# Optimization experiments

Hardware: AMD Instinct MI355X
Metric: run time of the kernel (lower is better)

Reference implementation:

```python
import jax, jax.numpy as jnp
import numpy as np

N_NODES = 50000

def setup_inputs() -> dict:
    key = jax.random.key(0)
    ks = jax.random.split(key, 8)
    d_in, d_h = 128, 128
    x = jax.random.normal(ks[0], (N_NODES, d_in), dtype=jnp.float32)
    edge_index = jax.random.randint(ks[1], (2, 800000), 0, N_NODES, dtype=jnp.int64)
    edge_pairs = jax.random.randint(ks[2], (1000000, 2), 0, N_NODES, dtype=jnp.int64)
    W_gcn = jax.random.normal(ks[3], (d_in, d_h), dtype=jnp.float32) / np.sqrt(d_in)
    b_gcn = jnp.zeros((d_h,), dtype=jnp.float32)
    W1 = jax.random.normal(ks[4], (2 * d_h, d_h), dtype=jnp.float32) / np.sqrt(2 * d_h)
    b1 = jnp.zeros((d_h,), dtype=jnp.float32)
    W2 = jax.random.normal(ks[5], (d_h, 1), dtype=jnp.float32) / np.sqrt(d_h)
    b2 = jnp.zeros((1,), dtype=jnp.float32)
    return {"x": x, "edge_index": edge_index, "edge_pairs": edge_pairs,
            "W_gcn": W_gcn, "b_gcn": b_gcn, "W1": W1, "b1": b1, "W2": W2, "b2": b2}

def gcn_conv(x, edge_index, W, b):
    # PyG GCNConv default: add self-loops, symmetric normalization.
    n = x.shape[0]
    loop = jnp.arange(n, dtype=edge_index.dtype)
    src = jnp.concatenate([edge_index[0], loop])  # [E+N]
    dst = jnp.concatenate([edge_index[1], loop])
    deg = jax.ops.segment_sum(jnp.ones(src.shape[0], dtype=x.dtype), dst, num_segments=n)
    dinv = jnp.where(deg > 0, jax.lax.rsqrt(deg), 0.0)
    norm = dinv[src] * dinv[dst]                  # [E+N]
    h = x @ W                                     # [N, H]
    agg = jax.ops.segment_sum(h[src] * norm[:, None], dst, num_segments=n)
    return agg + b

def reference(x, edge_index, edge_pairs, W_gcn, b_gcn, W1, b1, W2, b2):
    h = gcn_conv(x, edge_index, W_gcn, b_gcn)      # [N, H]
    e = jnp.concatenate([h[edge_pairs[:, 0]], h[edge_pairs[:, 1]]], axis=-1)  # [P, 2H]
    edge_logits = jax.nn.relu(e @ W1 + b1) @ W2 + b2  # [P, 1]
    return edge_logits, edge_pairs, h
```

## Files before the change

kernel.cpp:

```cpp
#include <hip/hip_runtime.h>
#include <hip/hip_fp16.h>

#define WG 256

typedef _Float16 f16;
typedef _Float16 hv2 __attribute__((ext_vector_type(2)));
typedef _Float16 f16x4 __attribute__((ext_vector_type(4)));
typedef _Float16 f16x8 __attribute__((ext_vector_type(8)));
typedef float f32x4 __attribute__((ext_vector_type(4)));

__global__ __launch_bounds__(WG) void k_misc0(const float* __restrict__ Wg,
                                              f16* __restrict__ Wgt,
                                              const float* __restrict__ W1,
                                              f16* __restrict__ W1t) {
    int b = blockIdx.x;
    if (b < 64) {
        int i = b * WG + threadIdx.x;
        int k = i & 127, nI = i >> 7;
        Wgt[i] = (f16)Wg[(size_t)k * 128 + nI];
    } else {
        int i = (b - 64) * WG + threadIdx.x;
        int k = i & 255, nI = i >> 8;
        W1t[i] = (f16)W1[(size_t)k * 128 + nI];
    }
}

__global__ __launch_bounds__(WG) void k_fusedA(const float* __restrict__ A,
                                               const f16* __restrict__ Wt,
                                               __half2* __restrict__ Out, int n,
                                               const int* __restrict__ dst,
                                               int* __restrict__ deg,
                                               int* __restrict__ rank, int e,
                                               const int* __restrict__ pairs,
                                               float* __restrict__ outp, int n4,
                                               int nmm, int necnt, int ncvt) {
    __shared__ __align__(16) char smem[64 * 136 * 2 + 128 * 136 * 2];
    int b = blockIdx.x, slot = b & 3, idx = b >> 2;
    int tid = threadIdx.x;
    if (slot == 1 || slot == 3) {
        int hid = idx * 2 + (slot >> 1);
        if (hid >= necnt) return;
        int i = hid * WG + tid;
        if (i < e) rank[i] = atomicAdd(&deg[dst[i]], 1);
        return;
    }
    if (slot == 2) {
        if (idx >= ncvt) return;
        int i = idx * WG + tid;
        if (i < n4) {
            int4 v = ((const int4*)pairs)[i];
            ((float4*)outp)[i] = make_float4((float)v.x, (float)v.y, (float)v.z, (float)v.w);
        }
        return;
    }
    if (idx >= nmm) return;
    f16(*As)[136] = (f16(*)[136])smem;
    f16(*Bs)[136] = (f16(*)[136])(smem + 64 * 136 * 2);
    const int row0 = idx * 64;
    for (int f = tid; f < 128 * 16; f += WG) {
        int r = f >> 4, c = f & 15;
        *(float4*)&Bs[r][c * 8] = ((const float4*)Wt)[r * 16 + c];
    }
    for (int f = tid; f < 64 * 32; f += WG) {
        int r = f >> 5, c = f & 31;
        float4 v = make_float4(0.f, 0.f, 0.f, 0.f);
        if (row0 + r < n) v = ((const float4*)A)[(size_t)(row0 + r) * 32 + c];
        *(f16x4*)&As[r][c * 4] = (f16x4){(f16)v.x, (f16)v.y, (f16)v.z, (f16)v.w};
    }
    __syncthreads();
    const int wv = tid >> 6, lane = tid & 63, m = lane & 15, quad = lane >> 4;
    f32x4 acc[8];
#pragma unroll
    for (int t = 0; t < 8; ++t) acc[t] = (f32x4){0.f, 0.f, 0.f, 0.f};
#pragma unroll
    for (int kk = 0; kk < 4; ++kk) {
        f16x8 af = *(f16x8*)&As[wv * 16 + m][kk * 32 + quad * 8];
#pragma unroll
        for (int t = 0; t < 8; ++t) {
            f16x8 bf = *(f16x8*)&Bs[t * 16 + m][kk * 32 + quad * 8];
            acc[t] = __builtin_amdgcn_mfma_f32_16x16x32_f16(af, bf, acc[t], 0, 0, 0);
        }
    }
#pragma unroll
    for (int r = 0; r < 4; ++r) {
        int row = row0 + wv * 16 + quad * 4 + r;
        if (row < n) {
#pragma unroll
            for (int t = 0; t < 4; ++t)
                Out[(size_t)row * 64 + t * 16 + m] =
                    __floats2half2_rn(acc[t][r], acc[t + 4][r]);
        }
    }
}

__global__ __launch_bounds__(WG) void k_scan1(const int* __restrict__ deg,
                                              float* __restrict__ dinv,
                                              int* __restrict__ base,
                                              int* __restrict__ bsum, int n) {
    __shared__ int t[WG];
    int tid = threadIdx.x;
    int i = blockIdx.x * WG + tid;
    int v = (i < n) ? deg[i] : 0;
    if (i < n) dinv[i] = rsqrtf((float)(v + 1));
    t[tid] = v;
    __syncthreads();
    for (int o = 1; o < WG; o <<= 1) {
        int add = (tid >= o) ? t[tid - o] : 0;
        __syncthreads();
        t[tid] += add;
        __syncthreads();
    }
    if (i < n) base[i] = t[tid] - v;
    if (tid == WG - 1) bsum[blockIdx.x] = t[WG - 1];
}

__global__ __launch_bounds__(WG) void k_scan23(int* __restrict__ base,
                                               const int* __restrict__ bsum,
                                               int n, int e, int nb) {
    __shared__ int t[WG];
    int tid = threadIdx.x;
    int v = (tid < nb) ? bsum[tid] : 0;
    t[tid] = v;
    __syncthreads();
    for (int o = 1; o < WG; o <<= 1) {
        int add = (tid >= o) ? t[tid - o] : 0;
        __syncthreads();
        t[tid] += add;
        __syncthreads();
    }
    int off = t[blockIdx.x] - ((blockIdx.x < nb) ? bsum[blockIdx.x] : 0);
    int i = blockIdx.x * WG + tid;
    if (i < n) {
        base[i] += off;
        if (i == n - 1) base[n] = e;
    }
}

__global__ __launch_bounds__(WG) void k_fill(const int* __restrict__ src,
                                             const int* __restrict__ dst,
                                             const int* __restrict__ base,
                                             const int* __restrict__ rank,
                                             int* __restrict__ esrc, int e) {
    int i = blockIdx.x * WG + threadIdx.x;
    if (i >= e) return;
    esrc[base[dst[i]] + rank[i]] = src[i];
}

__global__ __launch_bounds__(WG) void k_gather(const __half2* __restrict__ Hpk,
                                               const float* __restrict__ dinv,
                                               const float* __restrict__ bg,
                                               const int* __restrict__ base,
                                               const int* __restrict__ esrc,
                                               float* __restrict__ outh, int n) {
    int tid = threadIdx.x;
    int node = blockIdx.x * 16 + (tid >> 4);
    int sub = tid & 15;
    if (node >= n) return;
    float dv = dinv[node];
    int4 hh = *(const int4*)(Hpk + (size_t)node * 64 + 4 * sub);
    const int* hp = (const int*)&hh;
    float accl[4], acch[4];
#pragma unroll
    for (int k = 0; k < 4; ++k) {
        hv2 h = __builtin_bit_cast(hv2, hp[k]);
        accl[k] = (float)h[0] * dv;
        acch[k] = (float)h[1] * dv;
    }
    const int j = base[node], jend = base[node + 1];
    for (int j0 = j; j0 < jend; j0 += 8) {
        int s[8];
#pragma unroll
        for (int t = 0; t < 8; ++t) {
            int jt = j0 + t;
            s[t] = esrc[jt < jend ? jt : jend - 1];
        }
        float ds[8];
#pragma unroll
        for (int t = 0; t < 8; ++t) ds[t] = (j0 + t < jend) ? dinv[s[t]] : 0.f;
        int4 r[8];
#pragma unroll
        for (int t = 0; t < 8; ++t)
            r[t] = *(const int4*)(Hpk + (size_t)s[t] * 64 + 4 * sub);
#pragma unroll
        for (int t = 0; t < 8; ++t) {
            const int* pr = (const int*)&r[t];
#pragma unroll
            for (int k = 0; k < 4; ++k) {
                hv2 h = __builtin_bit_cast(hv2, pr[k]);
                accl[k] = fmaf((float)h[0], ds[t], accl[k]);
                acch[k] = fmaf((float)h[1], ds[t], acch[k]);
            }
        }
    }
    float4 blo = *(const float4*)(bg + 4 * sub);
    float4 bhi = *(const float4*)(bg + 4 * sub + 64);
    *(float4*)&outh[(size_t)node * 128 + 4 * sub] =
        make_float4(fmaf(accl[0], dv, blo.x), fmaf(accl[1], dv, blo.y),
                    fmaf(accl[2], dv, blo.z), fmaf(accl[3], dv, blo.w));
    *(float4*)&outh[(size_t)node * 128 + 64 + 4 * sub] =
        make_float4(fmaf(acch[0], dv, bhi.x), fmaf(acch[1], dv, bhi.y),
                    fmaf(acch[2], dv, bhi.z), fmaf(acch[3], dv, bhi.w));
}

__global__ __launch_bounds__(WG) void k_mm_uv(const float* __restrict__ A,
                                              const f16* __restrict__ W1t,
                                              const float* __restrict__ b1,
                                              __half2* __restrict__ Up,
                                              __half2* __restrict__ Vp, int n) {
    __shared__ f16 As[64][136];
    __shared__ f16 Bs[128][136];
    const int tid = threadIdx.x;
    const int row0 = blockIdx.x * 64;
    for (int f = tid; f < 64 * 32; f += WG) {
        int r = f >> 5, c = f & 31;
        float4 v = make_float4(0.f, 0.f, 0.f, 0.f);
        if (row0 + r < n) v = ((const float4*)A)[(size_t)(row0 + r) * 32 + c];
        *(f16x4*)&As[r][c * 4] = (f16x4){(f16)v.x, (f16)v.y, (f16)v.z, (f16)v.w};
    }
    const int wv = tid >> 6, lane = tid & 63, m = lane & 15, quad = lane >> 4;
    f32x4 acc[8];
#pragma unroll
    for (int ph = 0; ph < 2; ++ph) {
        if (ph) __syncthreads();
        for (int f = tid; f < 128 * 16; f += WG) {
            int r = f >> 4, c = f & 15;
            *(float4*)&Bs[r][c * 8] = *(const float4*)(W1t + (size_t)r * 256 + ph * 128 + c * 8);
        }
        __syncthreads();
#pragma unroll
        for (int t = 0; t < 8; ++t) acc[t] = (f32x4){0.f, 0.f, 0.f, 0.f};
#pragma unroll
        for (int kk = 0; kk < 4; ++kk) {
            f16x8 af = *(f16x8*)&As[wv * 16 + m][kk * 32 + quad * 8];
#pragma unroll
            for (int t = 0; t < 8; ++t) {
                f16x8 bf = *(f16x8*)&Bs[t * 16 + m][kk * 32 + quad * 8];
                acc[t] = __builtin_amdgcn_mfma_f32_16x16x32_f16(af, bf, acc[t], 0, 0, 0);
            }
        }
        __half2* Out = ph ? Vp : Up;
#pragma unroll
        for (int t = 0; t < 4; ++t) {
            float bl = 0.f, bh = 0.f;
            if (!ph) { bl = b1[t * 16 + m]; bh = b1[t * 16 + m + 64]; }
#pragma unroll
            for (int r = 0; r < 4; ++r) {
                int row = row0 + wv * 16 + quad * 4 + r;
                if (row < n)
                    Out[(size_t)row * 64 + t * 16 + m] =
                        __floats2half2_rn(acc[t][r] + bl, acc[t + 4][r] + bh);
            }
        }
    }
}

__global__ __launch_bounds__(WG) void k_pair16(const __half2* __restrict__ U,
                                               const __half2* __restrict__ V,
                                               const float* __restrict__ W2,
                                               const float* __restrict__ b2,
                                               const int* __restrict__ pairs,
                                               float* __restrict__ out_logit, int p) {
    int wv = (blockIdx.x * WG + threadIdx.x) >> 6;
    int lane = threadIdx.x & 63;
    int g = lane >> 4, sub = lane & 15;
    int qb = wv * 16 + g;
    if (qb >= p) return;
    int q0 = qb;
    int q1 = (qb + 4 < p) ? qb + 4 : qb;
    int q2 = (qb + 8 < p) ? qb + 8 : qb;
    int q3 = (qb + 12 < p) ? qb + 12 : qb;
    int a0 = pairs[2 * q0], b0 = pairs[2 * q0 + 1];
    int a1 = pairs[2 * q1], b1i = pairs[2 * q1 + 1];
    int a2 = pairs[2 * q2], b2i = pairs[2 * q2 + 1];
    int a3 = pairs[2 * q3], b3i = pairs[2 * q3 + 1];

    int4 u0 = *(const int4*)(U + (size_t)a0 * 64 + 4 * sub);
    int4 v0 = *(const int4*)(V + (size_t)b0 * 64 + 4 * sub);
    int4 u1 = *(const int4*)(U + (size_t)a1 * 64 + 4 * sub);
    int4 v1 = *(const int4*)(V + (size_t)b1i * 64 + 4 * sub);
    int4 u2 = *(const int4*)(U + (size_t)a2 * 64 + 4 * sub);
    int4 v2 = *(const int4*)(V + (size_t)b2i * 64 + 4 * sub);
    int4 u3 = *(const int4*)(U + (size_t)a3 * 64 + 4 * sub);
    int4 v3 = *(const int4*)(V + (size_t)b3i * 64 + 4 * sub);

    float4 w2lo = ((const float4*)W2)[sub];
    float4 w2hi = ((const float4*)(W2 + 64))[sub];
    hv2 w2h[4];
    w2h[0] = hv2{(f16)w2lo.x, (f16)w2hi.x};
    w2h[1] = hv2{(f16)w2lo.y, (f16)w2hi.y};
    w2h[2] = hv2{(f16)w2lo.z, (f16)w2hi.z};
    w2h[3] = hv2{(f16)w2lo.w, (f16)w2hi.w};

    const int* ui0 = (const int*)&u0;
    const int* vi0 = (const int*)&v0;
    const int* ui1 = (const int*)&u1;
    const int* vi1 = (const int*)&v1;
    const int* ui2 = (const int*)&u2;
    const int* vi2 = (const int*)&v2;
    const int* ui3 = (const int*)&u3;
    const int* vi3 = (const int*)&v3;

    const hv2 z2 = hv2{(f16)0.f, (f16)0.f};
    float p0 = 0.f, p1 = 0.f, p2 = 0.f, p3 = 0.f;
#pragma unroll
    for (int k = 0; k < 4; ++k) {
        hv2 s0 = __builtin_bit_cast(hv2, ui0[k]) + __builtin_bit_cast(hv2, vi0[k]);
        hv2 s1 = __builtin_bit_cast(hv2, ui1[k]) + __builtin_bit_cast(hv2, vi1[k]);
        hv2 s2 = __builtin_bit_cast(hv2, ui2[k]) + __builtin_bit_cast(hv2, vi2[k]);
        hv2 s3 = __builtin_bit_cast(hv2, ui3[k]) + __builtin_bit_cast(hv2, vi3[k]);
        p0 = __builtin_amdgcn_fdot2(__builtin_elementwise_max(s0, z2), w2h[k], p0, false);
        p1 = __builtin_amdgcn_fdot2(__builtin_elementwise_max(s1, z2), w2h[k], p1, false);
        p2 = __builtin_amdgcn_fdot2(__builtin_elementwise_max(s2, z2), w2h[k], p2, false);
        p3 = __builtin_amdgcn_fdot2(__builtin_elementwise_max(s3, z2), w2h[k], p3, false);
    }
#pragma unroll
    for (int m = 1; m < 16; m <<= 1) {
        p0 += __shfl_xor(p0, m, 64);
        p1 += __shfl_xor(p1, m, 64);
        p2 += __shfl_xor(p2, m, 64);
        p3 += __shfl_xor(p3, m, 64);
    }
    if (sub == 0) {
        float bb = b2[0];
        out_logit[q0] = p0 + bb;
        if (qb + 4 < p) out_logit[qb + 4] = p1 + bb;
        if (qb + 8 < p) out_logit[qb + 8] = p2 + bb;
        if (qb + 12 < p) out_logit[qb + 12] = p3 + bb;
    }
}

extern "C" void kernel_launch(void* const* d_in, const int* in_sizes, int n_in,
                              void* d_out, int out_size, void* d_ws, size_t ws_size,
                              hipStream_t stream) {
    const float* x     = (const float*)d_in[0];
    const int*   eidx  = (const int*)d_in[1];
    const int*   pairs = (const int*)d_in[2];
    const float* W_gcn = (const float*)d_in[3];
    const float* b_gcn = (const float*)d_in[4];
    const float* W1    = (const float*)d_in[5];
    const float* b1    = (const float*)d_in[6];
    const float* W2    = (const float*)d_in[7];
    const float* b2    = (const float*)d_in[8];

    const int N = in_sizes[0] / 128;
    const int E = in_sizes[1] / 2;
    const int P = in_sizes[2] / 2;
    const int* esrc_in = eidx;
    const int* edst_in = eidx + E;

    float* ws      = (float*)d_ws;
    int*   deg     = (int*)d_ws;
    float* dinv    = ws + 65536;
    int*   base    = (int*)(ws + 131072);
    int*   bsum    = (int*)(ws + 196608);
    f16*   Wt_gcn  = (f16*)(ws + 197120);
    f16*   W1t     = (f16*)(ws + 205312);
    int*   rank    = (int*)(ws + 221696);
    int*   ecsr    = rank + (size_t)E;
    __half2* Hpk   = (__half2*)(ecsr + (size_t)E);
    __half2* Upk   = Hpk + (size_t)N * 64;
    __half2* Vpk   = Upk + (size_t)N * 64;

    float* out_logit = (float*)d_out;
    float* out_pairs = out_logit + P;
    float* out_h     = out_logit + 3 * (size_t)P;

    const int nb    = (N + WG - 1) / WG;
    const int nmm   = (N + 63) / 64;
    const int necnt = (E + WG - 1) / WG;
    const int ncvt  = (P / 2 + WG - 1) / WG;
    int gmax = nmm;
    int h2 = (necnt + 1) / 2;
    if (h2 > gmax) gmax = h2;
    if (ncvt > gmax) gmax = ncvt;
    dim3 blk(WG);

    hipMemsetAsync(deg, 0, (size_t)N * 4, stream);
    k_misc0  <<<192, blk, 0, stream>>>(W_gcn, Wt_gcn, W1, W1t);
    k_fusedA <<<4 * gmax, blk, 0, stream>>>(x, Wt_gcn, Hpk, N,
                                            edst_in, deg, rank, E,
                                            pairs, out_pairs, P / 2,
                                            nmm, necnt, ncvt);
    k_scan1  <<<nb, blk, 0, stream>>>(deg, dinv, base, bsum, N);
    k_scan23 <<<nb, blk, 0, stream>>>(base, bsum, N, E, nb);
    k_fill   <<<necnt, blk, 0, stream>>>(esrc_in, edst_in, base, rank, ecsr, E);
    k_gather <<<(N + 15) / 16, blk, 0, stream>>>(Hpk, dinv, b_gcn, base, ecsr, out_h, N);
    k_mm_uv  <<<nmm, blk, 0, stream>>>(out_h, W1t, b1, Upk, Vpk, N);
    k_pair16 <<<(P + 63) / 64, blk, 0, stream>>>(Upk, Vpk, W2, b2, pairs, out_logit, P);
}
```

Measured before the change: 266.7 us.

## Bucket edge pairs by source-node slice to localize U gathers in pair kernel

After: 266.9 us. About the same (+0.1%).

```diff
diff --git a/kernel.cpp b/kernel.cpp
--- a/kernel.cpp
+++ b/kernel.cpp
@@ -33,6 +33,8 @@
                                                int* __restrict__ rank, int e,
                                                const int* __restrict__ pairs,
                                                float* __restrict__ outp, int n4,
+                                               int* __restrict__ pcount,
+                                               int* __restrict__ pboff, int slice,
                                                int nmm, int necnt, int ncvt) {
     __shared__ __align__(16) char smem[64 * 136 * 2 + 128 * 136 * 2];
     int b = blockIdx.x, slot = b & 3, idx = b >> 2;
@@ -46,11 +48,18 @@
     }
     if (slot == 2) {
         if (idx >= ncvt) return;
+        int* hist = (int*)smem;
+        if (tid < 8) hist[tid] = 0;
+        __syncthreads();
         int i = idx * WG + tid;
         if (i < n4) {
             int4 v = ((const int4*)pairs)[i];
             ((float4*)outp)[i] = make_float4((float)v.x, (float)v.y, (float)v.z, (float)v.w);
-        }
+            atomicAdd(&hist[v.x / slice], 1);
+            atomicAdd(&hist[v.z / slice], 1);
+        }
+        __syncthreads();
+        if (tid < 8) pboff[idx * 8 + tid] = atomicAdd(&pcount[tid], hist[tid]);
         return;
     }
     if (idx >= nmm) return;
@@ -202,15 +211,46 @@
                     fmaf(acch[2], dv, bhi.z), fmaf(acch[3], dv, bhi.w));
 }
 
-__global__ __launch_bounds__(WG) void k_mm_uv(const float* __restrict__ A,
-                                              const f16* __restrict__ W1t,
-                                              const float* __restrict__ b1,
-                                              __half2* __restrict__ Up,
-                                              __half2* __restrict__ Vp, int n) {
-    __shared__ f16 As[64][136];
-    __shared__ f16 Bs[128][136];
+__global__ __launch_bounds__(WG) void k_fusedE(const float* __restrict__ A,
+                                               const f16* __restrict__ W1t,
+                                               const float* __restrict__ b1,
+                                               __half2* __restrict__ Up,
+                                               __half2* __restrict__ Vp, int n, int nmm,
+                                               const int* __restrict__ pairs,
+                                               const int* __restrict__ pcount,
+                                               const int* __restrict__ pboff,
+                                               int2* __restrict__ plist2,
+                                               int n4, int ncvt, int slice) {
+    __shared__ __align__(16) char smem[64 * 136 * 2 + 128 * 136 * 2];
+    int b = blockIdx.x, slot = b & 1, idx = b >> 1;
     const int tid = threadIdx.x;
-    const int row0 = blockIdx.x * 64;
+    if (slot == 1) {
+        if (idx >= ncvt) return;
+        int* cnt8 = (int*)smem;
+        if (tid < 8) cnt8[tid] = 0;
+        __syncthreads();
+        int i = idx * WG + tid;
+        if (i < n4) {
+            int gb[8];
+            int run = 0;
+#pragma unroll
+            for (int k = 0; k < 8; ++k) { gb[k] = run; run += pcount[k]; }
+            int4 v = ((const int4*)pairs)[i];
+            int bk0 = v.x / slice;
+            int r0 = atomicAdd(&cnt8[bk0], 1);
+            int d0 = gb[bk0] + pboff[idx * 8 + bk0] + r0;
+            plist2[d0] = make_int2(v.y | ((v.x - bk0 * slice) << 16), 2 * i);
+            int bk1 = v.z / slice;
+            int r1 = atomicAdd(&cnt8[bk1], 1);
+            int d1 = gb[bk1] + pboff[idx * 8 + bk1] + r1;
+            plist2[d1] = make_int2(v.w | ((v.z - bk1 * slice) << 16), 2 * i + 1);
+        }
+        return;
+    }
+    if (idx >= nmm) return;
+    f16(*As)[136] = (f16(*)[136])smem;
+    f16(*Bs)[136] = (f16(*)[136])(smem + 64 * 136 * 2);
+    const int row0 = idx * 64;
     for (int f = tid; f < 64 * 32; f += WG) {
         int r = f >> 5, c = f & 31;
         float4 v = make_float4(0.f, 0.f, 0.f, 0.f);
@@ -254,34 +294,29 @@
     }
 }
 
-__global__ __launch_bounds__(WG) void k_pair16(const __half2* __restrict__ U,
-                                               const __half2* __restrict__ V,
-                                               const float* __restrict__ W2,
-                                               const float* __restrict__ b2,
-                                               const int* __restrict__ pairs,
-                                               float* __restrict__ out_logit, int p) {
-    int wv = (blockIdx.x * WG + threadIdx.x) >> 6;
-    int lane = threadIdx.x & 63;
-    int g = lane >> 4, sub = lane & 15;
-    int qb = wv * 16 + g;
-    if (qb >= p) return;
-    int q0 = qb;
-    int q1 = (qb + 4 < p) ? qb + 4 : qb;
-    int q2 = (qb + 8 < p) ? qb + 8 : qb;
-    int q3 = (qb + 12 < p) ? qb + 12 : qb;
-    int a0 = pairs[2 * q0], b0 = pairs[2 * q0 + 1];
-    int a1 = pairs[2 * q1], b1i = pairs[2 * q1 + 1];
-    int a2 = pairs[2 * q2], b2i = pairs[2 * q2 + 1];
-    int a3 = pairs[2 * q3], b3i = pairs[2 * q3 + 1];
-
-    int4 u0 = *(const int4*)(U + (size_t)a0 * 64 + 4 * sub);
-    int4 v0 = *(const int4*)(V + (size_t)b0 * 64 + 4 * sub);
-    int4 u1 = *(const int4*)(U + (size_t)a1 * 64 + 4 * sub);
-    int4 v1 = *(const int4*)(V + (size_t)b1i * 64 + 4 * sub);
-    int4 u2 = *(const int4*)(U + (size_t)a2 * 64 + 4 * sub);
-    int4 v2 = *(const int4*)(V + (size_t)b2i * 64 + 4 * sub);
-    int4 u3 = *(const int4*)(U + (size_t)a3 * 64 + 4 * sub);
-    int4 v3 = *(const int4*)(V + (size_t)b3i * 64 + 4 * sub);
+__global__ __launch_bounds__(WG) void k_pairx(const __half2* __restrict__ U,
+                                              const __half2* __restrict__ V,
+                                              const float* __restrict__ W2,
+                                              const float* __restrict__ b2,
+                                              const int* __restrict__ pcount,
+                                              const int2* __restrict__ plist2,
+                                              float* __restrict__ out_logit,
+                                              int slice) {
+    const int bkt = blockIdx.x & 7, blkid = blockIdx.x >> 3, NB = gridDim.x >> 3;
+    int gbase = 0, cnt;
+    {
+        int c[8];
+#pragma unroll
+        for (int k = 0; k < 8; ++k) c[k] = pcount[k];
+#pragma unroll
+        for (int k = 0; k < 8; ++k)
+            if (k < bkt) gbase += c[k];
+        cnt = c[bkt];
+    }
+    const int2* pl = plist2 + gbase;
+    const int abase = bkt * slice;
+    const int lane = threadIdx.x & 63, wv = threadIdx.x >> 6;
+    const int g = lane >> 4, sub = lane & 15;
 
     float4 w2lo = ((const float4*)W2)[sub];
     float4 w2hi = ((const float4*)(W2 + 64))[sub];
@@ -290,42 +325,64 @@
     w2h[1] = hv2{(f16)w2lo.y, (f16)w2hi.y};
     w2h[2] = hv2{(f16)w2lo.z, (f16)w2hi.z};
     w2h[3] = hv2{(f16)w2lo.w, (f16)w2hi.w};
-
-    const int* ui0 = (const int*)&u0;
-    const int* vi0 = (const int*)&v0;
-    const int* ui1 = (const int*)&u1;
-    const int* vi1 = (const int*)&v1;
-    const int* ui2 = (const int*)&u2;
-    const int* vi2 = (const int*)&v2;
-    const int* ui3 = (const int*)&u3;
-    const int* vi3 = (const int*)&v3;
-
+    const float bb = b2[0];
     const hv2 z2 = hv2{(f16)0.f, (f16)0.f};
-    float p0 = 0.f, p1 = 0.f, p2 = 0.f, p3 = 0.f;
-#pragma unroll
-    for (int k = 0; k < 4; ++k) {
-        hv2 s0 = __builtin_bit_cast(hv2, ui0[k]) + __builtin_bit_cast(hv2, vi0[k]);
-        hv2 s1 = __builtin_bit_cast(hv2, ui1[k]) + __builtin_bit_cast(hv2, vi1[k]);
-        hv2 s2 = __builtin_bit_cast(hv2, ui2[k]) + __builtin_bit_cast(hv2, vi2[k]);
-        hv2 s3 = __builtin_bit_cast(hv2, ui3[k]) + __builtin_bit_cast(hv2, vi3[k]);
-        p0 = __builtin_amdgcn_fdot2(__builtin_elementwise_max(s0, z2), w2h[k], p0, false);
-        p1 = __builtin_amdgcn_fdot2(__builtin_elementwise_max(s1, z2), w2h[k], p1, false);
-        p2 = __builtin_amdgcn_fdot2(__builtin_elementwise_max(s2, z2), w2h[k], p2, false);
-        p3 = __builtin_amdgcn_fdot2(__builtin_elementwise_max(s3, z2), w2h[k], p3, false);
-    }
-#pragma unroll
-    for (int m = 1; m < 16; m <<= 1) {
-        p0 += __shfl_xor(p0, m, 64);
-        p1 += __shfl_xor(p1, m, 64);
-        p2 += __shfl_xor(p2, m, 64);
-        p3 += __shfl_xor(p3, m, 64);
-    }
-    if (sub == 0) {
-        float bb = b2[0];
-        out_logit[q0] = p0 + bb;
-        if (qb + 4 < p) out_logit[qb + 4] = p1 + bb;
-        if (qb + 8 < p) out_logit[qb + 8] = p2 + bb;
-        if (qb + 12 < p) out_logit[qb + 12] = p3 + bb;
+
+    for (int pos = blkid * 64 + wv * 16; pos < cnt; pos += NB * 64) {
+        int q0 = pos + g;
+        if (q0 >= cnt) continue;
+        int q1 = (q0 + 4 < cnt) ? q0 + 4 : q0;
+        int q2 = (q0 + 8 < cnt) ? q0 + 8 : q0;
+        int q3 = (q0 + 12 < cnt) ? q0 + 12 : q0;
+        int2 e0 = pl[q0], e1 = pl[q1], e2 = pl[q2], e3 = pl[q3];
+        int a0 = abase + (e0.x >> 16), b0 = e0.x & 0xFFFF;
+        int a1 = abase + (e1.x >> 16), b1i = e1.x & 0xFFFF;
+        int a2 = abase + (e2.x >> 16), b2i = e2.x & 0xFFFF;
+        int a3 = abase + (e3.x >> 16), b3i = e3.x & 0xFFFF;
+
+        int4 u0 = *(const int4*)(U + (size_t)a0 * 64 + 4 * sub);
+        int4 v0 = *(const int4*)(V + (size_t)b0 * 64 + 4 * sub);
+        int4 u1 = *(const int4*)(U + (size_t)a1 * 64 + 4 * sub);
+        int4 v1 = *(const int4*)(V + (size_t)b1i * 64 + 4 * sub);
+        int4 u2 = *(const int4*)(U + (size_t)a2 * 64 + 4 * sub);
+        int4 v2 = *(const int4*)(V + (size_t)b2i * 64 + 4 * sub);
+        int4 u3 = *(const int4*)(U + (size_t)a3 * 64 + 4 * sub);
+        int4 v3 = *(const int4*)(V + (size_t)b3i * 64 + 4 * sub);
+
+        const int* ui0 = (const int*)&u0;
+        const int* vi0 = (const int*)&v0;
+        const int* ui1 = (const int*)&u1;
+        const int* vi1 = (const int*)&v1;
+        const int* ui2 = (const int*)&u2;
+        const int* vi2 = (const int*)&v2;
+        const int* ui3 = (const int*)&u3;
+        const int* vi3 = (const int*)&v3;
+
+        float p0 = 0.f, p1 = 0.f, p2 = 0.f, p3 = 0.f;
+#pragma unroll
+        for (int k = 0; k < 4; ++k) {
+            hv2 s0 = __builtin_bit_cast(hv2, ui0[k]) + __builtin_bit_cast(hv2, vi0[k]);
+            hv2 s1 = __builtin_bit_cast(hv2, ui1[k]) + __builtin_bit_cast(hv2, vi1[k]);
+            hv2 s2 = __builtin_bit_cast(hv2, ui2[k]) + __builtin_bit_cast(hv2, vi2[k]);
+            hv2 s3 = __builtin_bit_cast(hv2, ui3[k]) + __builtin_bit_cast(hv2, vi3[k]);
+            p0 = __builtin_amdgcn_fdot2(__builtin_elementwise_max(s0, z2), w2h[k], p0, false);
+            p1 = __builtin_amdgcn_fdot2(__builtin_elementwise_max(s1, z2), w2h[k], p1, false);
+            p2 = __builtin_amdgcn_fdot2(__builtin_elementwise_max(s2, z2), w2h[k], p2, false);
+            p3 = __builtin_amdgcn_fdot2(__builtin_elementwise_max(s3, z2), w2h[k], p3, false);
+        }
+#pragma unroll
+        for (int m = 1; m < 16; m <<= 1) {
+            p0 += __shfl_xor(p0, m, 64);
+            p1 += __shfl_xor(p1, m, 64);
+            p2 += __shfl_xor(p2, m, 64);
+            p3 += __shfl_xor(p3, m, 64);
+        }
+        if (sub == 0) {
+            out_logit[e0.y] = p0 + bb;
+            if (q0 + 4 < cnt) out_logit[e1.y] = p1 + bb;
+            if (q0 + 8 < cnt) out_logit[e2.y] = p2 + bb;
+            if (q0 + 12 < cnt) out_logit[e3.y] = p3 + bb;
+        }
     }
 }
 
@@ -347,19 +404,23 @@
     const int P = in_sizes[2] / 2;
     const int* esrc_in = eidx;
     const int* edst_in = eidx + E;
+    const int slice = (N + 7) / 8;
 
     float* ws      = (float*)d_ws;
     int*   deg     = (int*)d_ws;
+    int*   pcount  = (int*)d_ws + N;
     float* dinv    = ws + 65536;
     int*   base    = (int*)(ws + 131072);
     int*   bsum    = (int*)(ws + 196608);
     f16*   Wt_gcn  = (f16*)(ws + 197120);
     f16*   W1t     = (f16*)(ws + 205312);
-    int*   rank    = (int*)(ws + 221696);
+    int*   pboff   = (int*)(ws + 221696);
+    int*   rank    = (int*)(ws + 238080);
     int*   ecsr    = rank + (size_t)E;
     __half2* Hpk   = (__half2*)(ecsr + (size_t)E);
     __half2* Upk   = Hpk + (size_t)N * 64;
     __half2* Vpk   = Upk + (size_t)N * 64;
+    int2*  plist2  = (int2*)Hpk;
 
     float* out_logit = (float*)d_out;
     float* out_pairs = out_logit + P;
@@ -373,18 +434,23 @@
     int h2 = (necnt + 1) / 2;
     if (h2 > gmax) gmax = h2;
     if (ncvt > gmax) gmax = ncvt;
+    int emax = (nmm > ncvt) ? nmm : ncvt;
     dim3 blk(WG);
 
-    hipMemsetAsync(deg, 0, (size_t)N * 4, stream);
+    hipMemsetAsync(deg, 0, (size_t)N * 4 + 32, stream);
     k_misc0  <<<192, blk, 0, stream>>>(W_gcn, Wt_gcn, W1, W1t);
     k_fusedA <<<4 * gmax, blk, 0, stream>>>(x, Wt_gcn, Hpk, N,
                                             edst_in, deg, rank, E,
                                             pairs, out_pairs, P / 2,
+                                            pcount, pboff, slice,
                                             nmm, necnt, ncvt);
     k_scan1  <<<nb, blk, 0, stream>>>(deg, dinv, base, bsum, N);
     k_scan23 <<<nb, blk, 0, stream>>>(base, bsum, N, E, nb);
     k_fill   <<<necnt, blk, 0, stream>>>(esrc_in, edst_in, base, rank, ecsr, E);
     k_gather <<<(N + 15) / 16, blk, 0, stream>>>(Hpk, dinv, b_gcn, base, ecsr, out_h, N);
-    k_mm_uv  <<<nmm, blk, 0, stream>>>(out_h, W1t, b1, Upk, Vpk, N);
-    k_pair16 <<<(P + 63) / 64, blk, 0, stream>>>(Upk, Vpk, W2, b2, pairs, out_logit, P);
-}
+    k_fusedE <<<2 * emax, blk, 0, stream>>>(out_h, W1t, b1, Upk, Vpk, N, nmm,
+                                            pairs, pcount, pboff, plist2,
+                                            P / 2, ncvt, slice);
+    k_pairx  <<<4096, blk, 0, stream>>>(Upk, Vpk, W2, b2, pcount, plist2,
+                                        out_logit, slice);
+}
```
